# Optimization experiments

Measured on AMD Instinct MI355X. Metric: run time of the kernel, lower is better.

The kernel has to match this reference:

```python
import jax, jax.numpy as jnp
import numpy as np

B, S, H, T, W = 8, 512, 768, 4, 10
NEG = -1e9

def _u(key, shape, k):
    return jax.random.uniform(key, shape, jnp.float32, -k, k)

def setup_inputs():
    key = jax.random.key(0)
    ks = jax.random.split(key, 20)
    kh = float(1.0 / np.sqrt(H)); kt = float(1.0 / np.sqrt(T))
    return dict(
        embeddings=jax.random.normal(ks[0], (B, S, H), jnp.float32),
        l1f_wih=_u(ks[1], (4 * H, H), kh), l1f_whh=_u(ks[2], (4 * H, H), kh), l1f_b=_u(ks[3], (4 * H,), kh),
        l1r_wih=_u(ks[4], (4 * H, H), kh), l1r_whh=_u(ks[5], (4 * H, H), kh), l1r_b=_u(ks[6], (4 * H,), kh),
        attn_w=_u(ks[7], (3 * H,), kh), attn_b=_u(ks[8], (1,), kh),
        l2f_wih=_u(ks[9], (4 * T, 2 * H), kt), l2f_whh=_u(ks[10], (4 * T, T), kt), l2f_b=_u(ks[11], (4 * T,), kt),
        l2r_wih=_u(ks[12], (4 * T, 2 * H), kt), l2r_whh=_u(ks[13], (4 * T, T), kt), l2r_b=_u(ks[14], (4 * T,), kt),
        crf_start=0.1 * jax.random.normal(ks[15], (T,), jnp.float32),
        crf_end=0.1 * jax.random.normal(ks[16], (T,), jnp.float32),
        crf_trans=0.1 * jax.random.normal(ks[17], (T, T), jnp.float32),
        window_size=W,
    )

def _lstm_dir(x, w_ih, w_hh, b):
    # x: [B,S,D] -> [B,S,Hh]; torch gate order i,f,g,o
    Hh = w_hh.shape[1]
    bs = x.shape[0]
    xs = (jnp.einsum('bsd,gd->bsg', x, w_ih) + b).transpose(1, 0, 2)  # [S,B,4Hh]
    def step(carry, xt):
        h, c = carry
        g = xt + h @ w_hh.T
        i, f, gg, o = jnp.split(g, 4, axis=-1)
        c = jax.nn.sigmoid(f) * c + jax.nn.sigmoid(i) * jnp.tanh(gg)
        h = jax.nn.sigmoid(o) * jnp.tanh(c)
        return (h, c), h
    init = (jnp.zeros((bs, Hh), x.dtype), jnp.zeros((bs, Hh), x.dtype))
    _, hs = jax.lax.scan(step, init, xs)
    return hs.transpose(1, 0, 2)

def _bilstm(x, pf, pr):
    hf = _lstm_dir(x, *pf)
    hr = _lstm_dir(x[:, ::-1], *pr)[:, ::-1]
    return jnp.concatenate([hf, hr], axis=-1)

def _win_attn(h, w, b, win):
    # h: [B,S,D]; similarity(hi,hj) = w1.hi + w2.hj + w3.(hi*hj) + b
    bs, s, d = h.shape
    w1, w2, w3 = w[:d], w[d:2 * d], w[2 * d:]
    offs = jnp.arange(-win, win + 1)                      # [K]
    idx = jnp.arange(s)[:, None] + offs[None, :]          # [S,K]
    valid = (idx >= 0) & (idx < s)
    idxc = jnp.clip(idx, 0, s - 1)
    hw = h[:, idxc]                                       # [B,S,K,D]
    scores = (h @ w1)[:, :, None] \
        + jnp.einsum('bskd,d->bsk', hw, w2) \
        + jnp.einsum('bsd,bskd->bsk', h * w3, hw) + b[0]
    scores = jnp.where(valid[None], scores, NEG)
    aw = jax.nn.softmax(scores, axis=-1)                  # [B,S,K]
    return jnp.einsum('bsk,bskd->bsd', aw, hw)

def _viterbi(em, start, end, trans):
    # em: [B,S,T] -> tags [B,S]
    score0 = start[None] + em[:, 0]
    ems = em.transpose(1, 0, 2)[1:]                       # [S-1,B,T]
    def step(score, e_t):
        nxt = score[:, :, None] + trans[None]             # [B,Tprev,T]
        best = jnp.max(nxt, axis=1) + e_t
        bp = jnp.argmax(nxt, axis=1)
        return best, bp
    final, bps = jax.lax.scan(step, score0, ems)          # bps [S-1,B,T]
    final = final + end[None]
    last = jnp.argmax(final, axis=-1)                     # [B]
    def back(tag, bp):
        prev = jnp.take_along_axis(bp, tag[:, None], axis=1)[:, 0]
        return prev, prev
    _, tags_rev = jax.lax.scan(back, last, bps[::-1])
    return jnp.concatenate([tags_rev[::-1], last[None]], axis=0).transpose(1, 0)

def reference(embeddings, l1f_wih, l1f_whh, l1f_b, l1r_wih, l1r_whh, l1r_b,
              attn_w, attn_b, l2f_wih, l2f_whh, l2f_b, l2r_wih, l2r_whh, l2r_b,
              crf_start, crf_end, crf_trans, window_size):
    h1 = _bilstm(embeddings, (l1f_wih, l1f_whh, l1f_b), (l1r_wih, l1r_whh, l1r_b))
    d = h1.shape[-1] // 2
    hs = h1[..., :d] + h1[..., d:]                        # sum of directions [B,S,H]
    att = _win_attn(hs, attn_w, attn_b, int(window_size))
    x2 = jnp.concatenate([hs, att], axis=-1)              # [B,S,2H]
    h2 = _bilstm(x2, (l2f_wih, l2f_whh, l2f_b), (l2r_wih, l2r_whh, l2r_b))
    d2 = h2.shape[-1] // 2
    em = h2[..., :d2] + h2[..., d2:]                      # CRF emissions [B,S,T]
    tags = _viterbi(em, crf_start, crf_end, crf_trans)
    return tags, em
```

## Files before the change

### kernel.cpp

```cpp
#include <hip/hip_runtime.h>
#include <math.h>

#define SEQ 512
#define BATCH 8
#define HID 768
#define G4 3072
#define CHUNK 128
#define NEGV (-1000000000.0f)

typedef float v4f __attribute__((ext_vector_type(4)));
typedef float v2f __attribute__((ext_vector_type(2)));

__device__ __forceinline__ float sigm(float x) { return 1.0f / (1.0f + expf(-x)); }

__device__ __forceinline__ v2f fma2(v2f a, v2f b, v2f c) {
#if __has_builtin(__builtin_elementwise_fma)
  return __builtin_elementwise_fma(a, b, c);
#else
  v2f r; r.x = __builtin_fmaf(a.x, b.x, c.x); r.y = __builtin_fmaf(a.y, b.y, c.y);
  return r;
#endif
}

__device__ __forceinline__ float wred(float x) {
#pragma unroll
  for (int off = 32; off > 0; off >>= 1) x += __shfl_xor(x, off, 64);
  return x;
}

__device__ __forceinline__ void load2_f4_sc(const float* p0, const float* p1,
                                            v4f& a, v4f& b) {
  asm volatile("global_load_dwordx4 %0, %2, off sc0 sc1\n\t"
               "global_load_dwordx4 %1, %3, off sc0 sc1\n\t"
               "s_waitcnt vmcnt(0)"
               : "=&v"(a), "=&v"(b) : "v"(p0), "v"(p1) : "memory");
}
__device__ __forceinline__ int load_i_sc(const int* p) {
  int r;
  asm volatile("global_load_dword %0, %1, off sc0 sc1\n\ts_waitcnt vmcnt(0)"
               : "=v"(r) : "v"(p) : "memory");
  return r;
}
__device__ __forceinline__ void store_f_sc(float* p, float v) {
  asm volatile("global_store_dword %0, %1, off sc0 sc1" :: "v"(p), "v"(v) : "memory");
}
__device__ __forceinline__ void store_i_sc(int* p, int v) {
  asm volatile("global_store_dword %0, %1, off sc0 sc1" :: "v"(p), "v"(v) : "memory");
}

template <int CTRL, int RMASK>
__device__ __forceinline__ float dpp_add(float x) {
  int y = __builtin_amdgcn_update_dpp(0, __float_as_int(x), CTRL, RMASK, 0xF, false);
  return x + __int_as_float(y);
}
__device__ __forceinline__ float reduce32(float x) {
  x = dpp_add<0x121, 0xF>(x);
  x = dpp_add<0x122, 0xF>(x);
  x = dpp_add<0x124, 0xF>(x);
  x = dpp_add<0x128, 0xF>(x);
  x = dpp_add<0x142, 0xA>(x);
  return x;
}

__global__ void k_init(float* __restrict__ hbuf, int* __restrict__ flags) {
  int i = blockIdx.x * blockDim.x + threadIdx.x;
  if (i < 2 * 2 * BATCH * HID) hbuf[i] = 0.0f;
  if (i < 4096) flags[i] = 0;
}

__global__ __launch_bounds__(256) void k_proj1(
    const float* __restrict__ emb,
    const float* __restrict__ w_f, const float* __restrict__ b_f,
    const float* __restrict__ w_r, const float* __restrict__ b_r,
    float* __restrict__ xs_f, float* __restrict__ xs_r, int chunk) {
  __shared__ float As[16][132];
  __shared__ float Bs[16][132];
  const int tid = threadIdx.x;
  const int bn0 = blockIdx.x * 128;
  const int bb  = blockIdx.y;
  const int dir = blockIdx.z;
  const float* W    = dir ? w_r : w_f;
  const float* bias = dir ? b_r : b_f;
  float* xs = dir ? xs_r : xs_f;

  v2f acc2[8][4];
#pragma unroll
  for (int i = 0; i < 8; i++)
#pragma unroll
    for (int j = 0; j < 4; j++) acc2[i][j] = (v2f){0.0f, 0.0f};

  const int mload = tid & 127;
  const int kq0   = tid >> 7;
  const int tglob = dir ? (SEQ - 1 - (chunk * CHUNK + mload)) : (chunk * CHUNK + mload);
  const float* arow = emb + (size_t)(bb * SEQ + tglob) * HID;
  const float* brow = W + (size_t)(bn0 + mload) * HID;
  const int tm = tid & 15, tn = tid >> 4;

  for (int kt = 0; kt < HID; kt += 16) {
#pragma unroll
    for (int rep = 0; rep < 2; rep++) {
      int kq = kq0 + rep * 2;
      float4 a = *(const float4*)(arow + kt + kq * 4);
      As[kq * 4 + 0][mload] = a.x; As[kq * 4 + 1][mload] = a.y;
      As[kq * 4 + 2][mload] = a.z; As[kq * 4 + 3][mload] = a.w;
      float4 b = *(const float4*)(brow + kt + kq * 4);
      Bs[kq * 4 + 0][mload] = b.x; Bs[kq * 4 + 1][mload] = b.y;
      Bs[kq * 4 + 2][mload] = b.z; Bs[kq * 4 + 3][mload] = b.w;
    }
    __syncthreads();
#pragma unroll
    for (int k = 0; k < 16; k++) {
      float4 a0 = *(const float4*)&As[k][tm * 8];
      float4 a1 = *(const float4*)&As[k][tm * 8 + 4];
      float4 b0 = *(const float4*)&Bs[k][tn * 8];
      float4 b1 = *(const float4*)&Bs[k][tn * 8 + 4];
      float av[8] = {a0.x, a0.y, a0.z, a0.w, a1.x, a1.y, a1.z, a1.w};
      v2f bv2[4] = {{b0.x, b0.y}, {b0.z, b0.w}, {b1.x, b1.y}, {b1.z, b1.w}};
#pragma unroll
      for (int i = 0; i < 8; i++) {
        v2f avv = {av[i], av[i]};
#pragma unroll
        for (int jj = 0; jj < 4; jj++) acc2[i][jj] = fma2(avv, bv2[jj], acc2[i][jj]);
      }
    }
    __syncthreads();
  }
#pragma unroll
  for (int i = 0; i < 8; i++) {
    int row = tm * 8 + i;
    size_t base = (size_t)(bb * CHUNK + row) * G4 + bn0 + tn * 8;
#pragma unroll
    for (int jj = 0; jj < 4; jj++) {
      xs[base + 2 * jj]     = acc2[i][jj].x + bias[bn0 + tn * 8 + 2 * jj];
      xs[base + 2 * jj + 1] = acc2[i][jj].y + bias[bn0 + tn * 8 + 2 * jj + 1];
    }
  }
}

__global__ __launch_bounds__(384, 2) void k_rec1(
    const float* __restrict__ whh_f, const float* __restrict__ whh_r,
    const float* __restrict__ xs_f, const float* __restrict__ xs_r,
    float* __restrict__ hbuf, float* __restrict__ cbuf, int* __restrict__ flags,
    float* __restrict__ hf, float* __restrict__ hr, int t0, int init) {
  __shared__ float hlds[4 * HID];
  const int tid = threadIdx.x;
  const int bid = blockIdx.x;
  const int dir = bid >> 7;
  const int bh  = (bid >> 6) & 1;
  const int jb  = bid & 63;
  const int J0  = jb * 12;
  const int grp = dir * 2 + bh;
  const int g  = tid >> 5;
  const int kq = tid & 31;
  const int j  = J0 + g;

  const float* W  = dir ? whh_r : whh_f;
  const float* xs = dir ? xs_r  : xs_f;
  float* harr = dir ? hr : hf;

  float wreg[4][24];
#pragma unroll
  for (int gate = 0; gate < 4; gate++) {
#pragma unroll
    for (int q = 0; q < 6; q++) {
      *(v4f*)&wreg[gate][q * 4] =
          *(const v4f*)&W[(size_t)(gate * HID + j) * HID + q * 128 + kq * 4];
    }
  }

  float cc[4];
#pragma unroll
  for (int b = 0; b < 4; b++) cc[b] = 0.0f;
  if (!init && kq == 16) {
#pragma unroll
    for (int b = 0; b < 4; b++) cc[b] = cbuf[bid * 48 + g * 4 + b];
  }

  for (int stp = 0; stp < CHUNK; stp++) {
    const int s = t0 + stp;
    const int par = s & 1;

    float xsv[4][4];
    if (kq == 16) {
#pragma unroll
      for (int b = 0; b < 4; b++) {
        const size_t xbase = (size_t)((bh * 4 + b) * CHUNK + stp) * G4 + j;
#pragma unroll
        for (int gate = 0; gate < 4; gate++)
          xsv[b][gate] = xs[xbase + gate * HID];
      }
    }

    if (tid < 64) {
      const int* fp = flags + (grp * 64 + tid) * 16;
      while (load_i_sc(fp) < s) { __builtin_amdgcn_s_sleep(4); }
    }
    __syncthreads();

    {
      const float* src = hbuf + (size_t)((par * 2 + dir) * BATCH + bh * 4) * HID + tid * 8;
      v4f a, b4;
      load2_f4_sc(src, src + 4, a, b4);
      *(v4f*)&hlds[tid * 8]     = a;
      *(v4f*)&hlds[tid * 8 + 4] = b4;
    }
    __syncthreads();

    float acc[4][4];
#pragma unroll
    for (int gate = 0; gate < 4; gate++)
#pragma unroll
      for (int b = 0; b < 4; b++) acc[gate][b] = 0.0f;
#pragma unroll
    for (int b = 0; b < 4; b++) {
      float hk[24];
#pragma unroll
      for (int q = 0; q < 6; q++)
        *(v4f*)&hk[q * 4] = *(const v4f*)&hlds[b * HID + q * 128 + kq * 4];
#pragma unroll
      for (int gate = 0; gate < 4; gate++)
#pragma unroll
        for (int k = 0; k < 24; k++) acc[gate][b] += wreg[gate][k] * hk[k];
    }
#pragma unroll
    for (int gate = 0; gate < 4; gate++)
#pragma unroll
      for (int b = 0; b < 4; b++) acc[gate][b] = reduce32(acc[gate][b]);

    if (kq == 16) {
      const int t = dir ? (SEQ - 1 - s) : s;
#pragma unroll
      for (int b = 0; b < 4; b++) {
        const int bg = bh * 4 + b;
        float iv = acc[0][b] + xsv[b][0];
        float fv = acc[1][b] + xsv[b][1];
        float gv = acc[2][b] + xsv[b][2];
        float ov = acc[3][b] + xsv[b][3];
        cc[b] = sigm(fv) * cc[b] + sigm(iv) * tanhf(gv);
        float h = sigm(ov) * tanhf(cc[b]);
        store_f_sc(hbuf + (size_t)(((par ^ 1) * 2 + dir) * BATCH + bg) * HID + j, h);
        harr[(size_t)(bg * SEQ + t) * HID + j] = h;
      }
    }
    asm volatile("s_waitcnt vmcnt(0)" ::: "memory");
    __syncthreads();
    if (tid == 0) store_i_sc(flags + (grp * 64 + jb) * 16, s + 1);
  }
  if (kq == 16) {
#pragma unroll
    for (int b = 0; b < 4; b++) cbuf[bid * 48 + g * 4 + b] = cc[b];
  }
}

__global__ void k_sum(float* __restrict__ hf, const float* __restrict__ hr) {
  int i = blockIdx.x * 256 + threadIdx.x;
  float4 a = ((const float4*)hf)[i];
  float4 b = ((const float4*)hr)[i];
  a.x += b.x; a.y += b.y; a.z += b.z; a.w += b.w;
  ((float4*)hf)[i] = a;
}

__global__ __launch_bounds__(64) void k_attn(
    const float* __restrict__ hs, const float* __restrict__ attn_w,
    const float* __restrict__ attn_b, float* __restrict__ att) {
  const int l = threadIdx.x;
  const int s = blockIdx.x, b = blockIdx.y;
  const float* hrow = hs + (size_t)(b * SEQ + s) * HID;
  float v[12];
  float u1p = 0.0f;
#pragma unroll
  for (int jj = 0; jj < 12; jj++) {
    int d = l + 64 * jj;
    float x = hrow[d];
    u1p += x * attn_w[d];
    v[jj] = attn_w[HID + d] + x * attn_w[2 * HID + d];
  }
  float u1 = wred(u1p) + attn_b[0];
  float sc[21];
  for (int o = 0; o < 21; o++) {
    int s2 = s + o - 10;
    if (s2 >= 0 && s2 < SEQ) {
      const float* h2 = hs + (size_t)(b * SEQ + s2) * HID;
      float p = 0.0f;
#pragma unroll
      for (int jj = 0; jj < 12; jj++) p += h2[l + 64 * jj] * v[jj];
      sc[o] = wred(p) + u1;
    } else {
      sc[o] = NEGV;
    }
  }
  float m = sc[0];
#pragma unroll
  for (int o = 1; o < 21; o++) m = fmaxf(m, sc[o]);
  float sum = 0.0f;
#pragma unroll
  for (int o = 0; o < 21; o++) { sc[o] = expf(sc[o] - m); sum += sc[o]; }
  float inv = 1.0f / sum;
  float acc[12];
#pragma unroll
  for (int jj = 0; jj < 12; jj++) acc[jj] = 0.0f;
  for (int o = 0; o < 21; o++) {
    int s2 = s + o - 10;
    if (s2 < 0 || s2 >= SEQ) continue;
    float a = sc[o] * inv;
    const float* h2 = hs + (size_t)(b * SEQ + s2) * HID;
#pragma unroll
    for (int jj = 0; jj < 12; jj++) acc[jj] += a * h2[l + 64 * jj];
  }
  float* orow = att + (size_t)(b * SEQ + s) * HID;
#pragma unroll
  for (int jj = 0; jj < 12; jj++) orow[l + 64 * jj] = acc[jj];
}

__global__ __launch_bounds__(256) void k_proj2(
    const float* __restrict__ hs, const float* __restrict__ att,
    const float* __restrict__ w2f, const float* __restrict__ b2f,
    const float* __restrict__ w2r, const float* __restrict__ b2r,
    float* __restrict__ xs2) {
  __shared__ __align__(16) float x2[2 * HID];
  __shared__ float part[32][9];
  const int tid = threadIdx.x;
  const int s = blockIdx.x, b = blockIdx.y;
  size_t base = (size_t)(b * SEQ + s) * HID;
  for (int i = tid; i < 2 * HID; i += 256)
    x2[i] = (i < HID) ? hs[base + i] : att[base + i - HID];
  __syncthreads();
  const int gid = tid & 31, pp = tid >> 5;
  const int d = gid >> 4, g = gid & 15;
  const float4* w4 = (const float4*)((d ? w2r : w2f) + (size_t)g * (2 * HID));
  const float4* x4 = (const float4*)x2;
  float p = 0.0f;
  for (int e = pp * 48; e < pp * 48 + 48; e++) {
    float4 xv = x4[e];
    float4 wv = w4[e];
    p += xv.x * wv.x + xv.y * wv.y + xv.z * wv.z + xv.w * wv.w;
  }
  part[gid][pp] = p;
  __syncthreads();
  if (tid < 32) {
    float sumv = (d ? b2r : b2f)[g];
#pragma unroll
    for (int q = 0; q < 8; q++) sumv += part[gid][q];
    xs2[(size_t)((d * BATCH + b) * SEQ + s) * 16 + g] = sumv;
  }
}

__global__ __launch_bounds__(256) void k_rec2(
    const float* __restrict__ xs2,
    const float* __restrict__ whh_f, const float* __restrict__ whh_r,
    float* __restrict__ h2) {
  const int tid = threadIdx.x;
  const int lane = tid & 63;
  const int hb = (tid >> 6) * 4 + (lane >> 4);
  const int g = lane & 15;
  const int d = hb >> 3;
  const int base = lane & 48;
  const float* whh = (d ? whh_r : whh_f) + g * 4;
  const float w0 = whh[0], w1 = whh[1], w2 = whh[2], w3 = whh[3];
  const float* xrow = xs2 + (size_t)hb * SEQ * 16 + g;
  float c = 0.0f, h = 0.0f;
  float xv = xrow[(d ? (SEQ - 1) : 0) * 16];
  for (int st = 0; st < SEQ; st++) {
    const int t = d ? (SEQ - 1 - st) : st;
    const int tn = d ? (SEQ - 2 - st) : (st + 1);
    float xnext = (st + 1 < SEQ) ? xrow[tn * 16] : 0.0f;
    float h0 = __shfl(h, base + 0, 64);
    float h1 = __shfl(h, base + 1, 64);
    float h2v = __shfl(h, base + 2, 64);
    float h3 = __shfl(h, base + 3, 64);
    float gv = xv + w0 * h0 + w1 * h1 + w2 * h2v + w3 * h3;
    const int jj = g & 3;
    float iv = __shfl(gv, base + jj, 64);
    float fv = __shfl(gv, base + 4 + jj, 64);
    float gq = __shfl(gv, base + 8 + jj, 64);
    float ov = __shfl(gv, base + 12 + jj, 64);
    c = sigm(fv) * c + sigm(iv) * tanhf(gq);
    h = sigm(ov) * tanhf(c);
    if (g < 4) h2[((size_t)hb * SEQ + t) * 4 + g] = h;
    xv = xnext;
  }
}

__global__ void k_em(const float* __restrict__ h2, float* __restrict__ out) {
  int i = blockIdx.x * 256 + threadIdx.x;
  if (i < BATCH * SEQ * 4) out[BATCH * SEQ + i] = h2[i] + h2[BATCH * SEQ * 4 + i];
}

__global__ __launch_bounds__(32) void k_viterbi(
    float* __restrict__ out, const float* __restrict__ start,
    const float* __restrict__ endw, const float* __restrict__ trans) {
  __shared__ unsigned char bp[SEQ - 1][32];
  const int l = threadIdx.x;
  const int b = l >> 2, j = l & 3;
  const float* em = out + BATCH * SEQ;
  const float tr0 = trans[0 * 4 + j], tr1 = trans[1 * 4 + j];
  const float tr2 = trans[2 * 4 + j], tr3 = trans[3 * 4 + j];
  float score = start[j] + em[((size_t)b * SEQ + 0) * 4 + j];
  for (int t = 1; t < SEQ; t++) {
    float s0 = __shfl(score, b * 4 + 0, 64);
    float s1 = __shfl(score, b * 4 + 1, 64);
    float s2 = __shfl(score, b * 4 + 2, 64);
    float s3 = __shfl(score, b * 4 + 3, 64);
    float v0 = s0 + tr0, v1 = s1 + tr1, v2 = s2 + tr2, v3 = s3 + tr3;
    float best = v0; int arg = 0;
    if (v1 > best) { best = v1; arg = 1; }
    if (v2 > best) { best = v2; arg = 2; }
    if (v3 > best) { best = v3; arg = 3; }
    bp[t - 1][l] = (unsigned char)arg;
    score = best + em[((size_t)b * SEQ + t) * 4 + j];
  }
  score += endw[j];
  float f0 = __shfl(score, b * 4 + 0, 64);
  float f1 = __shfl(score, b * 4 + 1, 64);
  float f2 = __shfl(score, b * 4 + 2, 64);
  float f3 = __shfl(score, b * 4 + 3, 64);
  if (j == 0) {
    float bbv = f0; int last = 0;
    if (f1 > bbv) { bbv = f1; last = 1; }
    if (f2 > bbv) { bbv = f2; last = 2; }
    if (f3 > bbv) { bbv = f3; last = 3; }
    int tag = last;
    out[b * SEQ + (SEQ - 1)] = (float)tag;
    for (int t = SEQ - 2; t >= 0; t--) {
      tag = bp[t][b * 4 + tag];
      out[b * SEQ + t] = (float)tag;
    }
  }
}

extern "C" void kernel_launch(void* const* d_in, const int* in_sizes, int n_in,
                              void* d_out, int out_size, void* d_ws, size_t ws_size,
                              hipStream_t stream) {
  const float* emb      = (const float*)d_in[0];
  const float* l1f_wih  = (const float*)d_in[1];
  const float* l1f_whh  = (const float*)d_in[2];
  const float* l1f_b    = (const float*)d_in[3];
  const float* l1r_wih  = (const float*)d_in[4];
  const float* l1r_whh  = (const float*)d_in[5];
  const float* l1r_b    = (const float*)d_in[6];
  const float* attn_w   = (const float*)d_in[7];
  const float* attn_b   = (const float*)d_in[8];
  const float* l2f_wih  = (const float*)d_in[9];
  const float* l2f_whh  = (const float*)d_in[10];
  const float* l2f_b    = (const float*)d_in[11];
  const float* l2r_wih  = (const float*)d_in[12];
  const float* l2r_whh  = (const float*)d_in[13];
  const float* l2r_b    = (const float*)d_in[14];
  const float* crf_start= (const float*)d_in[15];
  const float* crf_end  = (const float*)d_in[16];
  const float* crf_trans= (const float*)d_in[17];

  float* ws = (float*)d_ws;
  const size_t NCH = (size_t)BATCH * CHUNK * G4;
  float* xs_f = ws;
  float* xs_r = xs_f + NCH;
  float* hf   = xs_r + NCH;
  float* hr   = hf + (size_t)BATCH * SEQ * HID;
  float* hbuf = hr + (size_t)BATCH * SEQ * HID;
  float* cbuf = hbuf + 2 * 2 * BATCH * HID;
  float* h2   = cbuf + 256 * 48;
  int*   flags= (int*)(h2 + 2 * BATCH * SEQ * 4);
  float* xs2  = xs_f;
  float* att  = xs_r;
  float* hs   = hf;

  k_init<<<dim3(96), dim3(256), 0, stream>>>(hbuf, flags);

  for (int c = 0; c < 4; c++) {
    k_proj1<<<dim3(24, 8, 2), dim3(256), 0, stream>>>(
        emb, l1f_wih, l1f_b, l1r_wih, l1r_b, xs_f, xs_r, c);
    k_rec1<<<dim3(256), dim3(384), 0, stream>>>(
        l1f_whh, l1r_whh, xs_f, xs_r, hbuf, cbuf, flags, hf, hr,
        c * CHUNK, c == 0 ? 1 : 0);
  }

  k_sum<<<dim3(3072), dim3(256), 0, stream>>>(hf, hr);
  k_attn<<<dim3(SEQ, BATCH), dim3(64), 0, stream>>>(hs, attn_w, attn_b, att);
  k_proj2<<<dim3(SEQ, BATCH), dim3(256), 0, stream>>>(
      hs, att, l2f_wih, l2f_b, l2r_wih, l2r_b, xs2);
  k_rec2<<<dim3(1), dim3(256), 0, stream>>>(xs2, l2f_whh, l2r_whh, h2);
  k_em<<<dim3(64), dim3(256), 0, stream>>>(h2, (float*)d_out);
  k_viterbi<<<dim3(1), dim3(32), 0, stream>>>((float*)d_out, crf_start, crf_end, crf_trans);
}
```

Baseline: 3.764 ms.

## Replace per-block flag barrier with sequence-tagged hidden-state packets in recurrence

The cross-block handoff in the layer-1 LSTM recurrence changes from separate flag words (wait for vmcnt, block barrier, flag store) to packets that carry the hidden values together with the step number. Consumers poll the packet data directly and exit once every tag reaches the current step. This drops the trailing s_waitcnt plus __syncthreads before publishing and the separate flag polling round-trip on each of the 512 steps. In exchange every thread polls 64 bytes per spin instead of one int, and the packet buffer carries twice as many bytes as the raw hidden state.

```diff
diff --git a/kernel.cpp b/kernel.cpp
--- a/kernel.cpp
+++ b/kernel.cpp
@@ -28,24 +28,18 @@
   return x;
 }
 
-__device__ __forceinline__ void load2_f4_sc(const float* p0, const float* p1,
-                                            v4f& a, v4f& b) {
-  asm volatile("global_load_dwordx4 %0, %2, off sc0 sc1\n\t"
-               "global_load_dwordx4 %1, %3, off sc0 sc1\n\t"
+__device__ __forceinline__ void store_pkt_sc(float* p, v4f v) {
+  asm volatile("global_store_dwordx4 %0, %1, off sc0 sc1" :: "v"(p), "v"(v) : "memory");
+}
+__device__ __forceinline__ void load4_pkt_sc(const float* p, v4f& a, v4f& b,
+                                             v4f& c, v4f& d) {
+  asm volatile("global_load_dwordx4 %0, %4, off sc0 sc1\n\t"
+               "global_load_dwordx4 %1, %4, off offset:16 sc0 sc1\n\t"
+               "global_load_dwordx4 %2, %4, off offset:32 sc0 sc1\n\t"
+               "global_load_dwordx4 %3, %4, off offset:48 sc0 sc1\n\t"
                "s_waitcnt vmcnt(0)"
-               : "=&v"(a), "=&v"(b) : "v"(p0), "v"(p1) : "memory");
-}
-__device__ __forceinline__ int load_i_sc(const int* p) {
-  int r;
-  asm volatile("global_load_dword %0, %1, off sc0 sc1\n\ts_waitcnt vmcnt(0)"
-               : "=v"(r) : "v"(p) : "memory");
-  return r;
-}
-__device__ __forceinline__ void store_f_sc(float* p, float v) {
-  asm volatile("global_store_dword %0, %1, off sc0 sc1" :: "v"(p), "v"(v) : "memory");
-}
-__device__ __forceinline__ void store_i_sc(int* p, int v) {
-  asm volatile("global_store_dword %0, %1, off sc0 sc1" :: "v"(p), "v"(v) : "memory");
+               : "=&v"(a), "=&v"(b), "=&v"(c), "=&v"(d)
+               : "v"(p) : "memory");
 }
 
 template <int CTRL, int RMASK>
@@ -62,10 +56,9 @@
   return x;
 }
 
-__global__ void k_init(float* __restrict__ hbuf, int* __restrict__ flags) {
+__global__ void k_init(float* __restrict__ pbuf) {
   int i = blockIdx.x * blockDim.x + threadIdx.x;
-  if (i < 2 * 2 * BATCH * HID) hbuf[i] = 0.0f;
-  if (i < 4096) flags[i] = 0;
+  if (i < 2 * 4 * 768 * 2 * 4) pbuf[i] = 0.0f;
 }
 
 __global__ __launch_bounds__(256) void k_proj1(
@@ -140,7 +133,7 @@
 __global__ __launch_bounds__(384, 2) void k_rec1(
     const float* __restrict__ whh_f, const float* __restrict__ whh_r,
     const float* __restrict__ xs_f, const float* __restrict__ xs_r,
-    float* __restrict__ hbuf, float* __restrict__ cbuf, int* __restrict__ flags,
+    float* __restrict__ pbuf, float* __restrict__ cbuf,
     float* __restrict__ hf, float* __restrict__ hr, int t0, int init) {
   __shared__ float hlds[4 * HID];
   const int tid = threadIdx.x;
@@ -191,18 +184,24 @@
       }
     }
 
-    if (tid < 64) {
-      const int* fp = flags + (grp * 64 + tid) * 16;
-      while (load_i_sc(fp) < s) { __builtin_amdgcn_s_sleep(4); }
+    v4f A0, A1, B0, B1;
+    {
+      const float* pb = pbuf + (size_t)(par * 4 + grp) * (768 * 2 * 4) + (size_t)tid * 16;
+      for (;;) {
+        load4_pkt_sc(pb, A0, A1, B0, B1);
+        if (__float_as_int(A0.z) >= s && __float_as_int(A1.z) >= s &&
+            __float_as_int(B0.z) >= s && __float_as_int(B1.z) >= s) break;
+        __builtin_amdgcn_s_sleep(8);
+      }
     }
     __syncthreads();
 
     {
-      const float* src = hbuf + (size_t)((par * 2 + dir) * BATCH + bh * 4) * HID + tid * 8;
-      v4f a, b4;
-      load2_f4_sc(src, src + 4, a, b4);
-      *(v4f*)&hlds[tid * 8]     = a;
-      *(v4f*)&hlds[tid * 8 + 4] = b4;
+      const int j2 = 2 * tid;
+      *(v2f*)&hlds[0 * HID + j2] = (v2f){A0.x, B0.x};
+      *(v2f*)&hlds[1 * HID + j2] = (v2f){A0.y, B0.y};
+      *(v2f*)&hlds[2 * HID + j2] = (v2f){A1.x, B1.x};
+      *(v2f*)&hlds[3 * HID + j2] = (v2f){A1.y, B1.y};
     }
     __syncthreads();
 
@@ -229,22 +228,24 @@
 
     if (kq == 16) {
       const int t = dir ? (SEQ - 1 - s) : s;
+      float hv[4];
 #pragma unroll
       for (int b = 0; b < 4; b++) {
-        const int bg = bh * 4 + b;
         float iv = acc[0][b] + xsv[b][0];
         float fv = acc[1][b] + xsv[b][1];
         float gv = acc[2][b] + xsv[b][2];
         float ov = acc[3][b] + xsv[b][3];
         cc[b] = sigm(fv) * cc[b] + sigm(iv) * tanhf(gv);
-        float h = sigm(ov) * tanhf(cc[b]);
-        store_f_sc(hbuf + (size_t)(((par ^ 1) * 2 + dir) * BATCH + bg) * HID + j, h);
-        harr[(size_t)(bg * SEQ + t) * HID + j] = h;
+        hv[b] = sigm(ov) * tanhf(cc[b]);
       }
-    }
-    asm volatile("s_waitcnt vmcnt(0)" ::: "memory");
-    __syncthreads();
-    if (tid == 0) store_i_sc(flags + (grp * 64 + jb) * 16, s + 1);
+      const float seqf = __int_as_float(s + 1);
+      float* wp = pbuf + (size_t)((par ^ 1) * 4 + grp) * (768 * 2 * 4) + (size_t)j * 8;
+      store_pkt_sc(wp,     (v4f){hv[0], hv[1], seqf, seqf});
+      store_pkt_sc(wp + 4, (v4f){hv[2], hv[3], seqf, seqf});
+#pragma unroll
+      for (int b = 0; b < 4; b++)
+        harr[(size_t)((bh * 4 + b) * SEQ + t) * HID + j] = hv[b];
+    }
   }
   if (kq == 16) {
 #pragma unroll
@@ -456,21 +457,20 @@
   float* xs_r = xs_f + NCH;
   float* hf   = xs_r + NCH;
   float* hr   = hf + (size_t)BATCH * SEQ * HID;
-  float* hbuf = hr + (size_t)BATCH * SEQ * HID;
-  float* cbuf = hbuf + 2 * 2 * BATCH * HID;
+  float* pbuf = hr + (size_t)BATCH * SEQ * HID;
+  float* cbuf = pbuf + 2 * 4 * 768 * 2 * 4;
   float* h2   = cbuf + 256 * 48;
-  int*   flags= (int*)(h2 + 2 * BATCH * SEQ * 4);
   float* xs2  = xs_f;
   float* att  = xs_r;
   float* hs   = hf;
 
-  k_init<<<dim3(96), dim3(256), 0, stream>>>(hbuf, flags);
+  k_init<<<dim3(192), dim3(256), 0, stream>>>(pbuf);
 
   for (int c = 0; c < 4; c++) {
     k_proj1<<<dim3(24, 8, 2), dim3(256), 0, stream>>>(
         emb, l1f_wih, l1f_b, l1r_wih, l1r_b, xs_f, xs_r, c);
     k_rec1<<<dim3(256), dim3(384), 0, stream>>>(
-        l1f_whh, l1r_whh, xs_f, xs_r, hbuf, cbuf, flags, hf, hr,
+        l1f_whh, l1r_whh, xs_f, xs_r, pbuf, cbuf, hf, hr,
         c * CHUNK, c == 0 ? 1 : 0);
   }
 
```

New measurement: 5.021 ms. 1.33x slower.
